# Kernel optimization log

Measured on AMD Instinct MI355X. Metric: run time of the kernel, lower is better.

The kernel has to match this reference:

```python
import jax, jax.numpy as jnp
import numpy as np

N_EMBED = 64
HEAD_SIZE = 64
B, T = 4096, 128

def setup_inputs() -> dict:
    key = jax.random.key(0)
    k0, k1, k2, k3 = jax.random.split(key, 4)
    x = jax.random.normal(k0, (B, T, N_EMBED), dtype=jnp.float32)
    # nn.Linear(N_EMBED, head_size, bias=False): weight shape [head_size, N_EMBED], y = x @ W.T
    Wq = jax.random.normal(k1, (HEAD_SIZE, N_EMBED), dtype=jnp.float32) * (1.0 / np.sqrt(N_EMBED))
    Wk = jax.random.normal(k2, (HEAD_SIZE, N_EMBED), dtype=jnp.float32) * (1.0 / np.sqrt(N_EMBED))
    Wv = jax.random.normal(k3, (HEAD_SIZE, N_EMBED), dtype=jnp.float32) * (1.0 / np.sqrt(N_EMBED))
    return {"x": x, "Wq": Wq, "Wk": Wk, "Wv": Wv}

def reference(x, Wq, Wk, Wv):
    # q,k,v: [B,T,H]
    q = jnp.einsum('btc,hc->bth', x, Wq)
    k = jnp.einsum('btc,hc->bth', x, Wk)
    v = jnp.einsum('btc,hc->bth', x, Wv)
    scale = HEAD_SIZE ** -0.5
    scores = jnp.einsum('bth,bsh->bts', q, k) * scale  # [B,T,T]
    Tdim = x.shape[1]
    causal = jnp.tril(jnp.ones((Tdim, Tdim), dtype=bool))
    scores = jnp.where(causal, scores, -jnp.inf)
    weights = jax.nn.softmax(scores, axis=-1)
    # dropout disabled (eval mode) for deterministic reference
    out = jnp.einsum('bts,bsh->bth', weights, v)  # [B,T,H]
    return out
```

## Files before the change

kernel.cpp:

```cpp
#include <hip/hip_runtime.h>
#include <hip/hip_bf16.h>

typedef float f4  __attribute__((ext_vector_type(4)));
typedef short s8v __attribute__((ext_vector_type(8)));
typedef short s4v __attribute__((ext_vector_type(4)));

#define MFMA16(a, b, c) __builtin_amdgcn_mfma_f32_16x16x32_bf16((a), (b), (c), 0, 0, 0)

__device__ __forceinline__ unsigned cvtpk(float a, float b) {
  __hip_bfloat162 h2 = __float22bfloat162_rn(make_float2(a, b));
  unsigned u;
  __builtin_memcpy(&u, &h2, 4);
  return u;
}
__device__ __forceinline__ float bf2f(unsigned short s) {
  union { unsigned u; float f; } x; x.u = ((unsigned)s) << 16; return x.f;
}
__device__ __forceinline__ s8v cvt8(const float* p) {
  float4 a = *(const float4*)p;
  float4 b = *(const float4*)(p + 4);
  union { unsigned u[4]; s8v v; } r;
  r.u[0] = cvtpk(a.x, a.y); r.u[1] = cvtpk(a.z, a.w);
  r.u[2] = cvtpk(b.x, b.y); r.u[3] = cvtpk(b.z, b.w);
  return r.v;
}
__device__ __forceinline__ s8v mk8(unsigned a0, unsigned a1, unsigned b0, unsigned b1) {
  union { unsigned u[4]; s8v v; } r;
  r.u[0] = a0; r.u[1] = a1; r.u[2] = b0; r.u[3] = b1;
  return r.v;
}
__device__ __forceinline__ s8v ld44(const short* p0, const short* p1) {
  s4v a = *(const s4v*)p0;
  s4v b = *(const s4v*)p1;
  s8v r;
  r[0] = a[0]; r[1] = a[1]; r[2] = a[2]; r[3] = a[3];
  r[4] = b[0]; r[5] = b[1]; r[6] = b[2]; r[7] = b[3];
  return r;
}

__global__ __launch_bounds__(256, 4)
void attn_head(const void* __restrict__ xg, const void* __restrict__ wqg,
               const void* __restrict__ wkg, const void* __restrict__ wvg,
               void* __restrict__ outg) {
  __shared__ __align__(16) short smem[16384];
  short* Ksm = smem;
  short* Vt  = smem + 8192;

  const int tid  = threadIdx.x;
  const int wave = tid >> 6;
  const int lane = tid & 63;
  const int c16  = lane & 15;
  const int quad = lane >> 4;
  const int b    = blockIdx.x;
  const int swz  = c16 << 2;

  int isbf;
  {
    const unsigned short* w = (const unsigned short*)wqg;
    float f = bf2f(w[lane]);
    float a = fabsf(f);
    int ok = (f == 0.0f || (a >= 1e-4f && a <= 1e4f)) ? 1 : 0;
    unsigned long long ball = __ballot(ok);
    isbf = (__popcll(ball) >= 58) ? 1 : 0;
  }

  const int mts[2] = {wave, 7 - wave};

  s8v xf[2][2];
  #pragma unroll
  for (int mi = 0; mi < 2; mi++) {
    const size_t base = (size_t)b * (128 * 64) + (size_t)(mts[mi] * 16 + c16) * 64;
    #pragma unroll
    for (int kt = 0; kt < 2; kt++) {
      const int off = kt * 32 + quad * 8;
      if (isbf) xf[mi][kt] = *(const s8v*)((const unsigned short*)xg + base + off);
      else      xf[mi][kt] = cvt8((const float*)xg + base + off);
    }
  }

  f4 QT[2][4];
  #pragma unroll
  for (int ht = 0; ht < 4; ht++) {
    s8v wqf[2], wkf[2], wvf[2];
    const int woff0 = (ht * 16 + c16) * 64 + quad * 8;
    #pragma unroll
    for (int kt = 0; kt < 2; kt++) {
      const int off = woff0 + kt * 32;
      if (isbf) {
        wqf[kt] = *(const s8v*)((const unsigned short*)wqg + off);
        wkf[kt] = *(const s8v*)((const unsigned short*)wkg + off);
        wvf[kt] = *(const s8v*)((const unsigned short*)wvg + off);
      } else {
        wqf[kt] = cvt8((const float*)wqg + off);
        wkf[kt] = cvt8((const float*)wkg + off);
        wvf[kt] = cvt8((const float*)wvg + off);
      }
    }
    #pragma unroll
    for (int mi = 0; mi < 2; mi++) {
      const int m = mts[mi];
      f4 z = {0.f, 0.f, 0.f, 0.f};
      f4 qt = z, kk = z, vv = z;
      qt = MFMA16(wqf[0], xf[mi][0], qt);  qt = MFMA16(wqf[1], xf[mi][1], qt);
      kk = MFMA16(wkf[0], xf[mi][0], kk);  kk = MFMA16(wkf[1], xf[mi][1], kk);
      vv = MFMA16(xf[mi][0], wvf[0], vv);  vv = MFMA16(xf[mi][1], wvf[1], vv);
      QT[mi][ht] = qt;
      {
        union { unsigned u[2]; s4v v; } pk;
        pk.u[0] = cvtpk(kk[0], kk[1]); pk.u[1] = cvtpk(kk[2], kk[3]);
        *(s4v*)(Ksm + (m * 16 + c16) * 64 + ((ht * 16 + quad * 4) ^ swz)) = pk.v;
      }
      {
        union { unsigned u[2]; s4v v; } pv;
        pv.u[0] = cvtpk(vv[0], vv[1]); pv.u[1] = cvtpk(vv[2], vv[3]);
        *(s4v*)(Vt + (ht * 16 + c16) * 128 + ((m * 16 + quad * 4) ^ swz)) = pv.v;
      }
    }
  }

  s8v qb[2][2];
  #pragma unroll
  for (int mi = 0; mi < 2; mi++)
    #pragma unroll
    for (int hp = 0; hp < 2; hp++)
      qb[mi][hp] = mk8(
          cvtpk(QT[mi][2*hp][0]   * 0.125f, QT[mi][2*hp][1]   * 0.125f),
          cvtpk(QT[mi][2*hp][2]   * 0.125f, QT[mi][2*hp][3]   * 0.125f),
          cvtpk(QT[mi][2*hp+1][0] * 0.125f, QT[mi][2*hp+1][1] * 0.125f),
          cvtpk(QT[mi][2*hp+1][2] * 0.125f, QT[mi][2*hp+1][3] * 0.125f));

  __syncthreads();

  #pragma unroll
  for (int mi = 0; mi < 2; mi++) {
    const int m = mts[mi];
    const int q4 = quad * 4;

    f4 S[8];
    #pragma unroll
    for (int nt = 0; nt < 8; nt++) {
      if (nt > m) continue;
      const short* kr = Ksm + (nt * 16 + c16) * 64;
      f4 s = {0.f, 0.f, 0.f, 0.f};
      s = MFMA16(ld44(kr + ((q4     ) ^ swz), kr + ((q4 + 16) ^ swz)), qb[mi][0], s);
      s = MFMA16(ld44(kr + ((q4 + 32) ^ swz), kr + ((q4 + 48) ^ swz)), qb[mi][1], s);
      S[nt] = s;
    }

    float sum = 0.f;
    #pragma unroll
    for (int nt = 0; nt < 8; nt++) {
      if (nt > m) continue;
      #pragma unroll
      for (int r = 0; r < 4; r++) {
        const bool keep = (nt < m) || (q4 + r <= c16);
        float e = keep ? __expf(S[nt][r]) : 0.0f;
        S[nt][r] = e;
        sum += e;
      }
    }
    sum += __shfl_xor(sum, 16);
    sum += __shfl_xor(sum, 32);
    const float inv = 1.0f / sum;

    unsigned ppk[8][2];
    #pragma unroll
    for (int nt = 0; nt < 8; nt++) {
      if (nt > m) continue;
      ppk[nt][0] = cvtpk(S[nt][0], S[nt][1]);
      ppk[nt][1] = cvtpk(S[nt][2], S[nt][3]);
    }

    f4 acc[4];
    #pragma unroll
    for (int ht = 0; ht < 4; ht++) { f4 z = {0.f,0.f,0.f,0.f}; acc[ht] = z; }
    const int nchunk = (m >> 1) + 1;
    #pragma unroll
    for (int kt = 0; kt < 4; kt++) {
      if (kt >= nchunk) continue;
      const bool hb = (2 * kt + 1) <= m;
      const s8v pb = mk8(ppk[2 * kt][0], ppk[2 * kt][1],
                         hb ? ppk[2 * kt + 1][0] : 0u,
                         hb ? ppk[2 * kt + 1][1] : 0u);
      #pragma unroll
      for (int ht = 0; ht < 4; ht++) {
        const short* vr = Vt + (ht * 16 + c16) * 128;
        const s8v va = ld44(vr + ((kt * 32 + q4     ) ^ swz),
                            vr + ((kt * 32 + q4 + 16) ^ swz));
        acc[ht] = MFMA16(va, pb, acc[ht]);
      }
    }

    if (isbf) {
      unsigned short* op = (unsigned short*)outg + (size_t)b * (128 * 64);
      #pragma unroll
      for (int ht = 0; ht < 4; ht++) {
        union { unsigned u[2]; s4v v; } o;
        o.u[0] = cvtpk(acc[ht][0] * inv, acc[ht][1] * inv);
        o.u[1] = cvtpk(acc[ht][2] * inv, acc[ht][3] * inv);
        *(s4v*)(op + (size_t)(m * 16 + c16) * 64 + ht * 16 + q4) = o.v;
      }
    } else {
      float* op = (float*)outg + (size_t)b * (128 * 64);
      #pragma unroll
      for (int ht = 0; ht < 4; ht++) {
        float4 o = {acc[ht][0] * inv, acc[ht][1] * inv,
                    acc[ht][2] * inv, acc[ht][3] * inv};
        *(float4*)(op + (size_t)(m * 16 + c16) * 64 + ht * 16 + q4) = o;
      }
    }
  }
}

extern "C" void kernel_launch(void* const* d_in, const int* in_sizes, int n_in,
                              void* d_out, int out_size, void* d_ws, size_t ws_size,
                              hipStream_t stream) {
  (void)d_ws; (void)ws_size; (void)in_sizes; (void)n_in; (void)out_size;
  attn_head<<<dim3(4096), dim3(256), 0, stream>>>(
      d_in[0], d_in[1], d_in[2], d_in[3], d_out);
}
```

Baseline: 323.8 us.

## Fuse QK scores, exp, and PV per key chunk to cut register pressure

Q is packed to bf16 right after projection instead of keeping fp32 Q tiles live until later. The attention loop now computes scores for two key tiles, exponentiates them and feeds them straight into the PV MFMAs, rather than materialising all 8 score tiles first. This lowers live VGPRs, which may help occupancy under launch_bounds(256,4) or reduce spills. In exchange it interleaves dependent MFMA chains and gives less independent work per chunk for latency hiding.

```diff
diff --git a/kernel.cpp b/kernel.cpp
--- a/kernel.cpp
+++ b/kernel.cpp
@@ -78,7 +78,7 @@
     }
   }
 
-  f4 QT[2][4];
+  unsigned qpk[2][4][2];
   #pragma unroll
   for (int ht = 0; ht < 4; ht++) {
     s8v wqf[2], wkf[2], wvf[2];
@@ -104,7 +104,8 @@
       qt = MFMA16(wqf[0], xf[mi][0], qt);  qt = MFMA16(wqf[1], xf[mi][1], qt);
       kk = MFMA16(wkf[0], xf[mi][0], kk);  kk = MFMA16(wkf[1], xf[mi][1], kk);
       vv = MFMA16(xf[mi][0], wvf[0], vv);  vv = MFMA16(xf[mi][1], wvf[1], vv);
-      QT[mi][ht] = qt;
+      qpk[mi][ht][0] = cvtpk(qt[0] * 0.125f, qt[1] * 0.125f);
+      qpk[mi][ht][1] = cvtpk(qt[2] * 0.125f, qt[3] * 0.125f);
       {
         union { unsigned u[2]; s4v v; } pk;
         pk.u[0] = cvtpk(kk[0], kk[1]); pk.u[1] = cvtpk(kk[2], kk[3]);
@@ -118,70 +119,55 @@
     }
   }
 
-  s8v qb[2][2];
-  #pragma unroll
-  for (int mi = 0; mi < 2; mi++)
-    #pragma unroll
-    for (int hp = 0; hp < 2; hp++)
-      qb[mi][hp] = mk8(
-          cvtpk(QT[mi][2*hp][0]   * 0.125f, QT[mi][2*hp][1]   * 0.125f),
-          cvtpk(QT[mi][2*hp][2]   * 0.125f, QT[mi][2*hp][3]   * 0.125f),
-          cvtpk(QT[mi][2*hp+1][0] * 0.125f, QT[mi][2*hp+1][1] * 0.125f),
-          cvtpk(QT[mi][2*hp+1][2] * 0.125f, QT[mi][2*hp+1][3] * 0.125f));
-
   __syncthreads();
 
   #pragma unroll
   for (int mi = 0; mi < 2; mi++) {
     const int m = mts[mi];
     const int q4 = quad * 4;
-
-    f4 S[8];
-    #pragma unroll
-    for (int nt = 0; nt < 8; nt++) {
-      if (nt > m) continue;
-      const short* kr = Ksm + (nt * 16 + c16) * 64;
-      f4 s = {0.f, 0.f, 0.f, 0.f};
-      s = MFMA16(ld44(kr + ((q4     ) ^ swz), kr + ((q4 + 16) ^ swz)), qb[mi][0], s);
-      s = MFMA16(ld44(kr + ((q4 + 32) ^ swz), kr + ((q4 + 48) ^ swz)), qb[mi][1], s);
-      S[nt] = s;
-    }
-
+    const s8v qb0 = mk8(qpk[mi][0][0], qpk[mi][0][1], qpk[mi][1][0], qpk[mi][1][1]);
+    const s8v qb1 = mk8(qpk[mi][2][0], qpk[mi][2][1], qpk[mi][3][0], qpk[mi][3][1]);
+
+    f4 acc[4];
+    #pragma unroll
+    for (int ht = 0; ht < 4; ht++) { f4 z = {0.f,0.f,0.f,0.f}; acc[ht] = z; }
     float sum = 0.f;
-    #pragma unroll
-    for (int nt = 0; nt < 8; nt++) {
-      if (nt > m) continue;
-      #pragma unroll
-      for (int r = 0; r < 4; r++) {
-        const bool keep = (nt < m) || (q4 + r <= c16);
-        float e = keep ? __expf(S[nt][r]) : 0.0f;
-        S[nt][r] = e;
-        sum += e;
-      }
-    }
-    sum += __shfl_xor(sum, 16);
-    sum += __shfl_xor(sum, 32);
-    const float inv = 1.0f / sum;
-
-    unsigned ppk[8][2];
-    #pragma unroll
-    for (int nt = 0; nt < 8; nt++) {
-      if (nt > m) continue;
-      ppk[nt][0] = cvtpk(S[nt][0], S[nt][1]);
-      ppk[nt][1] = cvtpk(S[nt][2], S[nt][3]);
-    }
-
-    f4 acc[4];
-    #pragma unroll
-    for (int ht = 0; ht < 4; ht++) { f4 z = {0.f,0.f,0.f,0.f}; acc[ht] = z; }
     const int nchunk = (m >> 1) + 1;
+
     #pragma unroll
     for (int kt = 0; kt < 4; kt++) {
       if (kt >= nchunk) continue;
-      const bool hb = (2 * kt + 1) <= m;
-      const s8v pb = mk8(ppk[2 * kt][0], ppk[2 * kt][1],
-                         hb ? ppk[2 * kt + 1][0] : 0u,
-                         hb ? ppk[2 * kt + 1][1] : 0u);
+      const int nt0 = 2 * kt, nt1 = 2 * kt + 1;
+      const bool hb = nt1 <= m;
+
+      f4 z = {0.f, 0.f, 0.f, 0.f};
+      f4 s0 = z, s1 = z;
+      {
+        const short* kr = Ksm + (nt0 * 16 + c16) * 64;
+        s0 = MFMA16(ld44(kr + ((q4     ) ^ swz), kr + ((q4 + 16) ^ swz)), qb0, s0);
+        s0 = MFMA16(ld44(kr + ((q4 + 32) ^ swz), kr + ((q4 + 48) ^ swz)), qb1, s0);
+      }
+      if (hb) {
+        const short* kr = Ksm + (nt1 * 16 + c16) * 64;
+        s1 = MFMA16(ld44(kr + ((q4     ) ^ swz), kr + ((q4 + 16) ^ swz)), qb0, s1);
+        s1 = MFMA16(ld44(kr + ((q4 + 32) ^ swz), kr + ((q4 + 48) ^ swz)), qb1, s1);
+      }
+      #pragma unroll
+      for (int r = 0; r < 4; r++) {
+        const bool k0 = (nt0 < m) || (q4 + r <= c16);
+        float e0 = k0 ? __expf(s0[r]) : 0.0f;
+        s0[r] = e0; sum += e0;
+      }
+      if (hb) {
+        #pragma unroll
+        for (int r = 0; r < 4; r++) {
+          const bool k1 = (nt1 < m) || (q4 + r <= c16);
+          float e1 = k1 ? __expf(s1[r]) : 0.0f;
+          s1[r] = e1; sum += e1;
+        }
+      }
+      const s8v pb = mk8(cvtpk(s0[0], s0[1]), cvtpk(s0[2], s0[3]),
+                         cvtpk(s1[0], s1[1]), cvtpk(s1[2], s1[3]));
       #pragma unroll
       for (int ht = 0; ht < 4; ht++) {
         const short* vr = Vt + (ht * 16 + c16) * 128;
@@ -190,6 +176,10 @@
         acc[ht] = MFMA16(va, pb, acc[ht]);
       }
     }
+
+    sum += __shfl_xor(sum, 16);
+    sum += __shfl_xor(sum, 32);
+    const float inv = 1.0f / sum;
 
     if (isbf) {
       unsigned short* op = (unsigned short*)outg + (size_t)b * (128 * 64);
```

After: 299.8 us. 7.4% less time.
